# Performance work log

Measured on AMD Instinct MI355X. Metric: run time of the kernel, lower is better.

The kernel has to match this reference:

```python
import jax, jax.numpy as jnp
import numpy as np

B, N, E, H = 4, 4096, 1024, 16
D = E // H            # head_dim = 64
P_DIM = 64            # proj_dim; feature dim = 2*P_DIM = 128
EPS = 1e-4


def setup_inputs() -> dict:
    key = jax.random.key(0)
    ks = jax.random.split(key, 9)
    x = jax.random.normal(ks[0], (B, N, E), jnp.float32)
    init = 0.02
    Wq = jax.random.normal(ks[1], (E, E), jnp.float32) * init
    Wk = jax.random.normal(ks[2], (E, E), jnp.float32) * init
    Wv = jax.random.normal(ks[3], (E, E), jnp.float32) * init
    Wo = jax.random.normal(ks[4], (E, E), jnp.float32) * init
    bq = jnp.zeros((E,), jnp.float32)
    bk = jnp.zeros((E,), jnp.float32)
    bv = jnp.zeros((E,), jnp.float32)
    bo = jnp.zeros((E,), jnp.float32)
    # orthogonal random projection matrix (proj_dim, head_dim), fixed (non-trainable)
    g = np.random.default_rng(0).normal(size=(P_DIM, D))
    P = jnp.asarray(np.linalg.qr(g)[0], jnp.float32)
    return dict(x=x, Wq=Wq, bq=bq, Wk=Wk, bk=bk, Wv=Wv, bv=bv, Wo=Wo, bo=bo, P=P)


def _heads(z):
    # (B, N, E) -> (B, H, N, D)
    return z.reshape(B, N, H, D).transpose(0, 2, 1, 3)


def _normalize(z):
    return z / (jnp.linalg.norm(z, axis=-1, keepdims=True) + EPS)


def reference(x, Wq, bq, Wk, bk, Wv, bv, Wo, bo, P):
    q = _heads(x @ Wq.T + bq)
    k = _heads(x @ Wk.T + bk)
    v = _heads(x @ Wv.T + bv)
    q = _normalize(q)
    k = _normalize(k)
    scale = H ** 0.25
    qp = jnp.einsum('bhnd,ed->bhne', q, P) * scale
    kp = jnp.einsum('bhnd,ed->bhne', k, P) * scale
    fscale = P_DIM ** (-0.5)   # x.shape[-1]**-0.5 with last dim = proj_dim
    qf = jnp.concatenate([jnp.sin(qp), jnp.cos(qp)], axis=-1) * fscale  # (B,H,N,2p)
    kf = jnp.concatenate([jnp.sin(kp), jnp.cos(kp)], axis=-1) * fscale
    # non-causal linear attention: q @ (k^T v)
    kv = jnp.einsum('bhme,bhmd->bhed', kf, v)          # (B,H,2p,D)
    o = jnp.einsum('bhne,bhed->bhnd', qf, kv)          # (B,H,N,D)
    o = o.transpose(0, 2, 1, 3).reshape(B, N, E)
    return o @ Wo.T + bo
```

## Files before the change

kernel.cpp:

```cpp
#include <hip/hip_runtime.h>
#include <hip/hip_bf16.h>
#include <stdint.h>


typedef __bf16 bf16x8 __attribute__((ext_vector_type(8)));
typedef float f32x4 __attribute__((ext_vector_type(4)));

#define AS1 __attribute__((address_space(1)))
#define AS3 __attribute__((address_space(3)))

__device__ __forceinline__ void gl2lds16(const void* g, void* l) {
    __builtin_amdgcn_global_load_lds((const AS1 void*)g, (AS3 void*)l, 16, 0, 0);
}

static constexpr int GM = 16384, GN = 1024, GK = 1024;

__global__ void detect_kernel(const unsigned short* __restrict__ x,
                              int* __restrict__ flag) {
    __shared__ int s;
    const int lane = threadIdx.x;
    if (lane == 0) s = 0;
    __syncthreads();
    int cnt = 0;
#pragma unroll
    for (int i = 0; i < 2; ++i) {
        const unsigned short u = x[i * 64 + lane];
        const int e = (u >> 7) & 0xFF;
        cnt += (e >= 117 && e <= 131) ? 1 : 0;
    }
    atomicAdd(&s, cnt);
    __syncthreads();
    if (lane == 0) *flag = (s >= 100) ? 1 : 0;
}

__global__ __launch_bounds__(256) void cvt_kernel(
    const void* __restrict__ src, __hip_bfloat16* __restrict__ dst,
    int n, const int* __restrict__ flag) {
    if (*flag) return;
    const int i = (blockIdx.x * 256 + threadIdx.x) * 8;
    if (i >= n) return;
    const float* s = (const float*)src + i;
    const float4 a = *(const float4*)s;
    const float4 b = *(const float4*)(s + 4);
    union { uint4 u; __hip_bfloat16 h[8]; } pk;
    pk.h[0] = __float2bfloat16(a.x); pk.h[1] = __float2bfloat16(a.y);
    pk.h[2] = __float2bfloat16(a.z); pk.h[3] = __float2bfloat16(a.w);
    pk.h[4] = __float2bfloat16(b.x); pk.h[5] = __float2bfloat16(b.y);
    pk.h[6] = __float2bfloat16(b.z); pk.h[7] = __float2bfloat16(b.w);
    *(uint4*)(dst + i) = pk.u;
}

__global__ __launch_bounds__(256) void gemm1_kernel(
    const void* __restrict__ Adirect,
    const __hip_bfloat16* __restrict__ Acvt,
    const void* __restrict__ Wr, const __hip_bfloat16* __restrict__ Wc,
    const void* __restrict__ bias_raw,
    void* __restrict__ Cout,
    const int* __restrict__ flag, int last)
{
    __shared__ unsigned short smem[2 * 128 * 64];
    unsigned short* sA = smem;
    unsigned short* sB = smem + 128 * 64;

    const int tid  = threadIdx.x;
    const int lane = tid & 63;
    const int w    = tid >> 6;
    const int wm   = w >> 1, wn = w & 1;
    const int lr   = lane & 15, lk = lane >> 4;

    const int id    = blockIdx.x;
    const int xcd   = id & 7;
    const int slot  = id >> 3;
    const int m0    = (xcd * 16 + (slot & 15)) * 128;
    const int n0    = (slot >> 4) * 128;
    const int fl    = *flag;

    const __hip_bfloat16* A = fl ? (const __hip_bfloat16*)Adirect : Acvt;
    const __hip_bfloat16* W = fl ? (const __hip_bfloat16*)Wr : Wc;

    f32x4 acc[4][4];
#pragma unroll
    for (int i = 0; i < 4; ++i)
#pragma unroll
        for (int j = 0; j < 4; ++j)
            acc[i][j] = (f32x4){0.f, 0.f, 0.f, 0.f};

    const __hip_bfloat16* Ab = A + (size_t)m0 * GK;
    const __hip_bfloat16* Wb = W + (size_t)n0 * GK;

    for (int k0 = 0; k0 < GK; k0 += 64) {
#pragma unroll
        for (int j = 0; j < 4; ++j) {
            const int chunk = j * 256 + tid;
            const int row   = chunk >> 3;
            const int c     = chunk & 7;
            const int cs    = c ^ (row & 7);
            gl2lds16(Ab + (size_t)row * GK + k0 + cs * 8,
                     (char*)sA + (j * 256 + w * 64) * 16);
            gl2lds16(Wb + (size_t)row * GK + k0 + cs * 8,
                     (char*)sB + (j * 256 + w * 64) * 16);
        }
        __syncthreads();
#pragma unroll
        for (int kk = 0; kk < 64; kk += 32) {
            const int jj = ((kk >> 3) + lk) ^ (lr & 7);
            bf16x8 af[4], bfr[4];
#pragma unroll
            for (int i = 0; i < 4; ++i)
                af[i] = *(const bf16x8*)&sA[(wm * 64 + i * 16 + lr) * 64 + jj * 8];
#pragma unroll
            for (int j = 0; j < 4; ++j)
                bfr[j] = *(const bf16x8*)&sB[(wn * 64 + j * 16 + lr) * 64 + jj * 8];
#pragma unroll
            for (int i = 0; i < 4; ++i)
#pragma unroll
                for (int j = 0; j < 4; ++j)
                    acc[i][j] = __builtin_amdgcn_mfma_f32_16x16x32_bf16(
                        af[i], bfr[j], acc[i][j], 0, 0, 0);
        }
        __syncthreads();
    }

    const bool f32out = (last != 0) && (fl == 0);
    if (f32out) {
#pragma unroll
        for (int j = 0; j < 4; ++j) {
            const int col = n0 + wn * 64 + j * 16 + lr;
            const float bv = ((const float*)bias_raw)[col];
#pragma unroll
            for (int i = 0; i < 4; ++i) {
                const int rbase = m0 + wm * 64 + i * 16 + lk * 4;
#pragma unroll
                for (int r = 0; r < 4; ++r)
                    ((float*)Cout)[(size_t)(rbase + r) * GN + col] = acc[i][j][r] + bv;
            }
        }
        return;
    }
    __hip_bfloat16* sC = (__hip_bfloat16*)smem;
#pragma unroll
    for (int j = 0; j < 4; ++j) {
        const int col = wn * 64 + j * 16 + lr;
        const float bv = fl ? __bfloat162float(((const __hip_bfloat16*)bias_raw)[n0 + col])
                            : ((const float*)bias_raw)[n0 + col];
        const int c2 = col >> 3, o = col & 7;
#pragma unroll
        for (int i = 0; i < 4; ++i) {
            const int rb = wm * 64 + i * 16 + lk * 4;
#pragma unroll
            for (int r = 0; r < 4; ++r) {
                const int row = rb + r;
                sC[row * 128 + (c2 ^ (row & 7)) * 8 + o] = __float2bfloat16(acc[i][j][r] + bv);
            }
        }
    }
    __syncthreads();
    {
        const int row = tid >> 1, hf = tid & 1;
        __hip_bfloat16* dst = (__hip_bfloat16*)Cout + (size_t)(m0 + row) * GN + n0 + hf * 64;
#pragma unroll
        for (int q = 0; q < 8; ++q) {
            const int cc = (hf * 8 + q) ^ (row & 7);
            *(uint4*)(dst + q * 8) = *(const uint4*)&sC[row * 128 + cc * 8];
        }
    }
}

__global__ __launch_bounds__(256, 2) void gemm2_kernel(
    const void* __restrict__ Adirect,
    const __hip_bfloat16* __restrict__ Acvt,
    const void* __restrict__ W0r, const __hip_bfloat16* __restrict__ W0c,
    const void* __restrict__ W1r, const __hip_bfloat16* __restrict__ W1c,
    const void* __restrict__ b0r, const void* __restrict__ b1r,
    void* __restrict__ o0, void* __restrict__ o1,
    const int* __restrict__ flag)
{
    __shared__ unsigned short smem[3 * 128 * 64];
    unsigned short* sA  = smem;
    unsigned short* sB0 = smem + 128 * 64;
    unsigned short* sB1 = smem + 2 * 128 * 64;

    const int tid  = threadIdx.x;
    const int lane = tid & 63;
    const int w    = tid >> 6;
    const int wm   = w >> 1, wn = w & 1;
    const int lr   = lane & 15, lk = lane >> 4;

    const int id    = blockIdx.x;
    const int xcd   = id & 7;
    const int slot  = id >> 3;
    const int m0    = (xcd * 16 + (slot & 15)) * 128;
    const int n0    = (slot >> 4) * 128;
    const int fl    = *flag;

    const __hip_bfloat16* A  = fl ? (const __hip_bfloat16*)Adirect : Acvt;
    const __hip_bfloat16* W0 = fl ? (const __hip_bfloat16*)W0r : W0c;
    const __hip_bfloat16* W1 = fl ? (const __hip_bfloat16*)W1r : W1c;

    f32x4 acc[2][4][4];
#pragma unroll
    for (int t = 0; t < 2; ++t)
#pragma unroll
        for (int i = 0; i < 4; ++i)
#pragma unroll
            for (int j = 0; j < 4; ++j)
                acc[t][i][j] = (f32x4){0.f, 0.f, 0.f, 0.f};

    const __hip_bfloat16* Ab  = A + (size_t)m0 * GK;
    const __hip_bfloat16* W0b = W0 + (size_t)n0 * GK;
    const __hip_bfloat16* W1b = W1 + (size_t)n0 * GK;

    for (int k0 = 0; k0 < GK; k0 += 64) {
#pragma unroll
        for (int j = 0; j < 4; ++j) {
            const int chunk = j * 256 + tid;
            const int row   = chunk >> 3;
            const int c     = chunk & 7;
            const int cs    = c ^ (row & 7);
            const size_t go = (size_t)row * GK + k0 + cs * 8;
            const int lo = (j * 256 + w * 64) * 16;
            gl2lds16(Ab  + go, (char*)sA  + lo);
            gl2lds16(W0b + go, (char*)sB0 + lo);
            gl2lds16(W1b + go, (char*)sB1 + lo);
        }
        __syncthreads();
#pragma unroll
        for (int kk = 0; kk < 64; kk += 32) {
            const int jj = ((kk >> 3) + lk) ^ (lr & 7);
            bf16x8 af[4], b0f[4], b1f[4];
#pragma unroll
            for (int i = 0; i < 4; ++i)
                af[i] = *(const bf16x8*)&sA[(wm * 64 + i * 16 + lr) * 64 + jj * 8];
#pragma unroll
            for (int j = 0; j < 4; ++j)
                b0f[j] = *(const bf16x8*)&sB0[(wn * 64 + j * 16 + lr) * 64 + jj * 8];
#pragma unroll
            for (int j = 0; j < 4; ++j)
                b1f[j] = *(const bf16x8*)&sB1[(wn * 64 + j * 16 + lr) * 64 + jj * 8];
#pragma unroll
            for (int i = 0; i < 4; ++i)
#pragma unroll
                for (int j = 0; j < 4; ++j) {
                    acc[0][i][j] = __builtin_amdgcn_mfma_f32_16x16x32_bf16(
                        af[i], b0f[j], acc[0][i][j], 0, 0, 0);
                    acc[1][i][j] = __builtin_amdgcn_mfma_f32_16x16x32_bf16(
                        af[i], b1f[j], acc[1][i][j], 0, 0, 0);
                }
        }
        __syncthreads();
    }

    __hip_bfloat16* sC = (__hip_bfloat16*)smem;
#pragma unroll
    for (int t = 0; t < 2; ++t) {
        const void* bias_raw = t ? b1r : b0r;
        void* Cout = t ? o1 : o0;
#pragma unroll
        for (int j = 0; j < 4; ++j) {
            const int col = wn * 64 + j * 16 + lr;
            const float bv = fl ? __bfloat162float(((const __hip_bfloat16*)bias_raw)[n0 + col])
                                : ((const float*)bias_raw)[n0 + col];
            const int c2 = col >> 3, o = col & 7;
#pragma unroll
            for (int i = 0; i < 4; ++i) {
                const int rb = wm * 64 + i * 16 + lk * 4;
#pragma unroll
                for (int r = 0; r < 4; ++r) {
                    const int row = rb + r;
                    sC[row * 128 + (c2 ^ (row & 7)) * 8 + o] =
                        __float2bfloat16(acc[t][i][j][r] + bv);
                }
            }
        }
        __syncthreads();
        {
            const int row = tid >> 1, hf = tid & 1;
            __hip_bfloat16* dst = (__hip_bfloat16*)Cout + (size_t)(m0 + row) * GN + n0 + hf * 64;
#pragma unroll
            for (int q = 0; q < 8; ++q) {
                const int cc = (hf * 8 + q) ^ (row & 7);
                *(uint4*)(dst + q * 8) = *(const uint4*)&sC[row * 128 + cc * 8];
            }
        }
        __syncthreads();
    }
}

__device__ __forceinline__ void load_P(const void* Praw, int f,
                                       __hip_bfloat16* sP, int tid) {
    const int e = tid >> 2, q = tid & 3;
    union { uint4 u[2]; __hip_bfloat16 h[16]; } pk;
    if (f) {
        pk.u[0] = *(const uint4*)((const __hip_bfloat16*)Praw + e * 64 + q * 16);
        pk.u[1] = *(const uint4*)((const __hip_bfloat16*)Praw + e * 64 + q * 16 + 8);
    } else {
        const float* ps = (const float*)Praw + e * 64 + q * 16;
#pragma unroll
        for (int j = 0; j < 16; ++j) pk.h[j] = __float2bfloat16(ps[j]);
    }
    *(uint4*)&sP[e * 72 + q * 16]     = pk.u[0];
    *(uint4*)&sP[e * 72 + q * 16 + 8] = pk.u[1];
}

__device__ __forceinline__ float sumsq16(uint4 a, uint4 b) {
    union { uint4 u; __hip_bfloat16 h[8]; } x0, x1;
    x0.u = a; x1.u = b;
    float ss = 0.f;
#pragma unroll
    for (int j = 0; j < 8; ++j) {
        float v0 = __bfloat162float(x0.h[j]); ss += v0 * v0;
        float v1 = __bfloat162float(x1.h[j]); ss += v1 * v1;
    }
    return ss;
}

__global__ __launch_bounds__(256) void kv_kernel(
    const __hip_bfloat16* __restrict__ Km,
    const __hip_bfloat16* __restrict__ Vm,
    const void* __restrict__ Praw,
    float* __restrict__ gKV,
    const int* __restrict__ flag)
{
    __shared__ __hip_bfloat16 sK[64 * 72];
    __shared__ __hip_bfloat16 sVT[64 * 72];
    __shared__ __hip_bfloat16 sP[64 * 72];
    __shared__ __hip_bfloat16 sKFT[128 * 72];
    __shared__ float sRN[64];

    const int tid  = threadIdx.x;
    const int lane = tid & 63;
    const int w    = tid >> 6;
    const int lr   = lane & 15, lk = lane >> 4;
    const int bh   = blockIdx.y;
    const int b    = bh >> 4, h = bh & 15;
    const int nst  = blockIdx.x * 256;
    const int f    = *flag;
    const int n    = tid >> 2, q2 = tid & 3;

    load_P(Praw, f, sP, tid);

    f32x4 acck[2][4];
#pragma unroll
    for (int i = 0; i < 2; ++i)
#pragma unroll
        for (int j = 0; j < 4; ++j)
            acck[i][j] = (f32x4){0.f, 0.f, 0.f, 0.f};

    size_t base = ((size_t)(b * 4096 + nst + n)) * 1024 + h * 64 + q2 * 16;
    uint4 ka = *(const uint4*)(Km + base), kb = *(const uint4*)(Km + base + 8);
    uint4 va = *(const uint4*)(Vm + base), vb = *(const uint4*)(Vm + base + 8);

    for (int s = 0; s < 4; ++s) {
        __syncthreads();
        *(uint4*)&sK[n * 72 + q2 * 16]     = ka;
        *(uint4*)&sK[n * 72 + q2 * 16 + 8] = kb;
        {
            union { uint4 u[2]; __hip_bfloat16 h[16]; } vv;
            vv.u[0] = va; vv.u[1] = vb;
#pragma unroll
            for (int j = 0; j < 16; ++j) sVT[(q2 * 16 + j) * 72 + n] = vv.h[j];
        }
        {
            float ss = sumsq16(ka, kb);
            ss += __shfl_xor(ss, 1, 64);
            ss += __shfl_xor(ss, 2, 64);
            if (q2 == 0) sRN[n] = 2.0f / (sqrtf(ss) + 1e-4f);
        }
        if (s < 3) {
            base = ((size_t)(b * 4096 + nst + (s + 1) * 64 + n)) * 1024 + h * 64 + q2 * 16;
            ka = *(const uint4*)(Km + base); kb = *(const uint4*)(Km + base + 8);
            va = *(const uint4*)(Vm + base); vb = *(const uint4*)(Vm + base + 8);
        }
        {
            bf16x8 afr0 = *(const bf16x8*)&sK[(w * 16 + lr) * 72 + lk * 8];
            bf16x8 afr1 = *(const bf16x8*)&sK[(w * 16 + lr) * 72 + 32 + lk * 8];
            float rn[4];
#pragma unroll
            for (int r = 0; r < 4; ++r) rn[r] = sRN[w * 16 + lk * 4 + r];
#pragma unroll
            for (int eb = 0; eb < 4; ++eb) {
                f32x4 pa = (f32x4){0.f, 0.f, 0.f, 0.f};
                bf16x8 b0 = *(const bf16x8*)&sP[(eb * 16 + lr) * 72 + lk * 8];
                bf16x8 b1 = *(const bf16x8*)&sP[(eb * 16 + lr) * 72 + 32 + lk * 8];
                pa = __builtin_amdgcn_mfma_f32_16x16x32_bf16(afr0, b0, pa, 0, 0, 0);
                pa = __builtin_amdgcn_mfma_f32_16x16x32_bf16(afr1, b1, pa, 0, 0, 0);
                const int col = eb * 16 + lr;
#pragma unroll
                for (int r = 0; r < 4; ++r) {
                    const int row = w * 16 + lk * 4 + r;
                    float sv, cv;
                    __sincosf(pa[r] * rn[r], &sv, &cv);
                    sKFT[col * 72 + row]        = __float2bfloat16(sv * 0.125f);
                    sKFT[(col + 64) * 72 + row] = __float2bfloat16(cv * 0.125f);
                }
            }
        }
        __syncthreads();
#pragma unroll
        for (int ks = 0; ks < 2; ++ks) {
            bf16x8 a2[2], b2[4];
            a2[0] = *(const bf16x8*)&sKFT[(w * 16 + lr) * 72 + ks * 32 + lk * 8];
            a2[1] = *(const bf16x8*)&sKFT[((w + 4) * 16 + lr) * 72 + ks * 32 + lk * 8];
#pragma unroll
            for (int db = 0; db < 4; ++db)
                b2[db] = *(const bf16x8*)&sVT[(db * 16 + lr) * 72 + ks * 32 + lk * 8];
#pragma unroll
            for (int i = 0; i < 2; ++i)
#pragma unroll
                for (int db = 0; db < 4; ++db)
                    acck[i][db] = __builtin_amdgcn_mfma_f32_16x16x32_bf16(
                        a2[i], b2[db], acck[i][db], 0, 0, 0);
        }
    }

    float* out = gKV + (size_t)bh * 8192;
#pragma unroll
    for (int i = 0; i < 2; ++i)
#pragma unroll
        for (int db = 0; db < 4; ++db)
#pragma unroll
            for (int r = 0; r < 4; ++r) {
                const int e = (w + 4 * i) * 16 + lk * 4 + r;
                const int d = db * 16 + lr;
                atomicAdd(out + e * 64 + d, acck[i][db][r]);
            }
}

__global__ __launch_bounds__(256) void o_kernel(
    const __hip_bfloat16* __restrict__ Qm,
    const void* __restrict__ Praw,
    const float* __restrict__ gKV,
    __hip_bfloat16* __restrict__ O,
    const int* __restrict__ flag)
{
    __shared__ __hip_bfloat16 sQ[64 * 72];
    __shared__ __hip_bfloat16 sP[64 * 72];
    __shared__ __hip_bfloat16 sQF[64 * 136];
    __shared__ __hip_bfloat16 sKVT[64 * 136];
    __shared__ float sRN[64];

    const int tid  = threadIdx.x;
    const int lane = tid & 63;
    const int w    = tid >> 6;
    const int lr   = lane & 15, lk = lane >> 4;
    const int bh   = blockIdx.y;
    const int b    = bh >> 4, h = bh & 15;
    const int nst  = blockIdx.x * 256;
    const int f    = *flag;
    const int n    = tid >> 2, q2 = tid & 3;

    load_P(Praw, f, sP, tid);
    {
        const float* kvsrc = gKV + (size_t)bh * 8192;
        for (int t = tid; t < 8192; t += 256) {
            const int e = t >> 6, d = t & 63;
            sKVT[d * 136 + e] = __float2bfloat16(kvsrc[t]);
        }
    }

    size_t base = ((size_t)(b * 4096 + nst + n)) * 1024 + h * 64 + q2 * 16;
    uint4 qa = *(const uint4*)(Qm + base), qb = *(const uint4*)(Qm + base + 8);

    __syncthreads();

    for (int s = 0; s < 4; ++s) {
        const int gn0 = nst + s * 64;
        *(uint4*)&sQ[n * 72 + q2 * 16]     = qa;
        *(uint4*)&sQ[n * 72 + q2 * 16 + 8] = qb;
        {
            float ss = sumsq16(qa, qb);
            ss += __shfl_xor(ss, 1, 64);
            ss += __shfl_xor(ss, 2, 64);
            if (q2 == 0) sRN[n] = 2.0f / (sqrtf(ss) + 1e-4f);
        }
        if (s < 3) {
            base = ((size_t)(b * 4096 + nst + (s + 1) * 64 + n)) * 1024 + h * 64 + q2 * 16;
            qa = *(const uint4*)(Qm + base); qb = *(const uint4*)(Qm + base + 8);
        }
        {
            bf16x8 afr0 = *(const bf16x8*)&sQ[(w * 16 + lr) * 72 + lk * 8];
            bf16x8 afr1 = *(const bf16x8*)&sQ[(w * 16 + lr) * 72 + 32 + lk * 8];
            float rn[4];
#pragma unroll
            for (int r = 0; r < 4; ++r) rn[r] = sRN[w * 16 + lk * 4 + r];
#pragma unroll
            for (int eb = 0; eb < 4; ++eb) {
                f32x4 pa = (f32x4){0.f, 0.f, 0.f, 0.f};
                bf16x8 b0 = *(const bf16x8*)&sP[(eb * 16 + lr) * 72 + lk * 8];
                bf16x8 b1 = *(const bf16x8*)&sP[(eb * 16 + lr) * 72 + 32 + lk * 8];
                pa = __builtin_amdgcn_mfma_f32_16x16x32_bf16(afr0, b0, pa, 0, 0, 0);
                pa = __builtin_amdgcn_mfma_f32_16x16x32_bf16(afr1, b1, pa, 0, 0, 0);
                const int col = eb * 16 + lr;
#pragma unroll
                for (int r = 0; r < 4; ++r) {
                    const int row = w * 16 + lk * 4 + r;
                    float sv, cv;
                    __sincosf(pa[r] * rn[r], &sv, &cv);
                    sQF[row * 136 + col]      = __float2bfloat16(sv * 0.125f);
                    sQF[row * 136 + 64 + col] = __float2bfloat16(cv * 0.125f);
                }
            }
        }
        f32x4 oacc[4];
#pragma unroll
        for (int nb = 0; nb < 4; ++nb) oacc[nb] = (f32x4){0.f, 0.f, 0.f, 0.f};
#pragma unroll
        for (int ks = 0; ks < 4; ++ks) {
            bf16x8 aa = *(const bf16x8*)&sQF[(w * 16 + lr) * 136 + ks * 32 + lk * 8];
#pragma unroll
            for (int nb = 0; nb < 4; ++nb) {
                bf16x8 bb = *(const bf16x8*)&sKVT[(nb * 16 + lr) * 136 + ks * 32 + lk * 8];
                oacc[nb] = __builtin_amdgcn_mfma_f32_16x16x32_bf16(aa, bb, oacc[nb], 0, 0, 0);
            }
        }
#pragma unroll
        for (int nb = 0; nb < 4; ++nb)
#pragma unroll
            for (int r = 0; r < 4; ++r)
                sQ[(w * 16 + lk * 4 + r) * 72 + nb * 16 + lr] =
                    __float2bfloat16(oacc[nb][r]);
        {
            uint4 o0 = *(uint4*)&sQ[n * 72 + q2 * 16];
            uint4 o1 = *(uint4*)&sQ[n * 72 + q2 * 16 + 8];
            const size_t obase = ((size_t)(b * 4096 + gn0 + n)) * 1024 + h * 64 + q2 * 16;
            *(uint4*)(O + obase)     = o0;
            *(uint4*)(O + obase + 8) = o1;
        }
    }
}

extern "C" void kernel_launch(void* const* d_in, const int* in_sizes, int n_in,
                              void* d_out, int out_size, void* d_ws, size_t ws_size,
                              hipStream_t stream)
{
    (void)in_sizes; (void)n_in; (void)out_size; (void)ws_size;
    const void* x  = d_in[0];
    const void* Wq = d_in[1];
    const void* bq = d_in[2];
    const void* Wk = d_in[3];
    const void* bk = d_in[4];
    const void* Wv = d_in[5];
    const void* bv = d_in[6];
    const void* Wo = d_in[7];
    const void* bo = d_in[8];
    const void* P  = d_in[9];

    constexpr size_t XE = (size_t)GM * GN;
    constexpr size_t WE = (size_t)GN * GK;
    constexpr size_t KVE = (size_t)64 * 128 * 64;

    __hip_bfloat16* xb  = (__hip_bfloat16*)d_ws;
    __hip_bfloat16* wqb = xb + XE;
    __hip_bfloat16* wkb = wqb + WE;
    __hip_bfloat16* wvb = wkb + WE;
    __hip_bfloat16* wob = wvb + WE;
    __hip_bfloat16* R1  = wob + WE;
    __hip_bfloat16* R2  = R1 + XE;
    float* gKV = (float*)(R2 + XE);
    int* flag  = (int*)(gKV + KVE);

    dim3 blk(256);
    hipLaunchKernelGGL(detect_kernel, dim3(1), dim3(64), 0, stream,
                       (const unsigned short*)x, flag);
    hipMemsetAsync(gKV, 0, KVE * sizeof(float), stream);

    hipLaunchKernelGGL(cvt_kernel, dim3(8192), blk, 0, stream, x,  xb,  (int)XE, flag);
    hipLaunchKernelGGL(cvt_kernel, dim3(512),  blk, 0, stream, Wq, wqb, (int)WE, flag);
    hipLaunchKernelGGL(cvt_kernel, dim3(512),  blk, 0, stream, Wk, wkb, (int)WE, flag);
    hipLaunchKernelGGL(cvt_kernel, dim3(512),  blk, 0, stream, Wv, wvb, (int)WE, flag);
    hipLaunchKernelGGL(cvt_kernel, dim3(512),  blk, 0, stream, Wo, wob, (int)WE, flag);

    hipLaunchKernelGGL(gemm2_kernel, dim3(1024), blk, 0, stream,
                       x, xb, Wk, wkb, Wv, wvb, bk, bv, R1, R2, flag);
    hipLaunchKernelGGL(kv_kernel, dim3(16, 64), blk, 0, stream, R1, R2, P, gKV, flag);
    hipLaunchKernelGGL(gemm1_kernel, dim3(1024), blk, 0, stream,
                       x, xb, Wq, wqb, bq, R2, flag, 0);
    hipLaunchKernelGGL(o_kernel, dim3(16, 64), blk, 0, stream, R2, P, gKV, R1, flag);
    hipLaunchKernelGGL(gemm1_kernel, dim3(1024), blk, 0, stream,
                       R1, R1, Wo, wob, bo, d_out, flag, 1);
}
```

Baseline: 404.5 us.

## Use 256x128 tiles in single GEMMs and replace KV atomics with slab reduction

```diff
diff --git a/kernel.cpp b/kernel.cpp
--- a/kernel.cpp
+++ b/kernel.cpp
@@ -14,6 +14,7 @@
 }
 
 static constexpr int GM = 16384, GN = 1024, GK = 1024;
+static constexpr int KV_SLABS = 8;
 
 __global__ void detect_kernel(const unsigned short* __restrict__ x,
                               int* __restrict__ flag) {
@@ -50,7 +51,7 @@
     *(uint4*)(dst + i) = pk.u;
 }
 
-__global__ __launch_bounds__(256) void gemm1_kernel(
+__global__ __launch_bounds__(256, 2) void gemm1m2_kernel(
     const void* __restrict__ Adirect,
     const __hip_bfloat16* __restrict__ Acvt,
     const void* __restrict__ Wr, const __hip_bfloat16* __restrict__ Wc,
@@ -58,9 +59,10 @@
     void* __restrict__ Cout,
     const int* __restrict__ flag, int last)
 {
-    __shared__ unsigned short smem[2 * 128 * 64];
-    unsigned short* sA = smem;
-    unsigned short* sB = smem + 128 * 64;
+    __shared__ unsigned short smem[3 * 128 * 64];
+    unsigned short* sA0 = smem;
+    unsigned short* sA1 = smem + 128 * 64;
+    unsigned short* sB  = smem + 2 * 128 * 64;
 
     const int tid  = threadIdx.x;
     const int lane = tid & 63;
@@ -68,25 +70,28 @@
     const int wm   = w >> 1, wn = w & 1;
     const int lr   = lane & 15, lk = lane >> 4;
 
-    const int id    = blockIdx.x;
-    const int xcd   = id & 7;
-    const int slot  = id >> 3;
-    const int m0    = (xcd * 16 + (slot & 15)) * 128;
-    const int n0    = (slot >> 4) * 128;
-    const int fl    = *flag;
+    const int id   = blockIdx.x;
+    const int xcd  = id & 7;
+    const int s    = id >> 3;
+    const int m0   = (xcd * 8 + (s & 7)) * 256;
+    const int n0   = (s >> 3) * 128;
+    const int fl   = *flag;
 
     const __hip_bfloat16* A = fl ? (const __hip_bfloat16*)Adirect : Acvt;
     const __hip_bfloat16* W = fl ? (const __hip_bfloat16*)Wr : Wc;
 
-    f32x4 acc[4][4];
-#pragma unroll
-    for (int i = 0; i < 4; ++i)
-#pragma unroll
-        for (int j = 0; j < 4; ++j)
-            acc[i][j] = (f32x4){0.f, 0.f, 0.f, 0.f};
-
-    const __hip_bfloat16* Ab = A + (size_t)m0 * GK;
-    const __hip_bfloat16* Wb = W + (size_t)n0 * GK;
+    f32x4 acc[2][4][4];
+#pragma unroll
+    for (int t = 0; t < 2; ++t)
+#pragma unroll
+        for (int i = 0; i < 4; ++i)
+#pragma unroll
+            for (int j = 0; j < 4; ++j)
+                acc[t][i][j] = (f32x4){0.f, 0.f, 0.f, 0.f};
+
+    const __hip_bfloat16* Ab0 = A + (size_t)m0 * GK;
+    const __hip_bfloat16* Ab1 = A + (size_t)(m0 + 128) * GK;
+    const __hip_bfloat16* Wb  = W + (size_t)n0 * GK;
 
     for (int k0 = 0; k0 < GK; k0 += 64) {
 #pragma unroll
@@ -95,28 +100,35 @@
             const int row   = chunk >> 3;
             const int c     = chunk & 7;
             const int cs    = c ^ (row & 7);
-            gl2lds16(Ab + (size_t)row * GK + k0 + cs * 8,
-                     (char*)sA + (j * 256 + w * 64) * 16);
-            gl2lds16(Wb + (size_t)row * GK + k0 + cs * 8,
-                     (char*)sB + (j * 256 + w * 64) * 16);
+            const size_t go = (size_t)row * GK + k0 + cs * 8;
+            const int lo = (j * 256 + w * 64) * 16;
+            gl2lds16(Ab0 + go, (char*)sA0 + lo);
+            gl2lds16(Ab1 + go, (char*)sA1 + lo);
+            gl2lds16(Wb  + go, (char*)sB  + lo);
         }
         __syncthreads();
 #pragma unroll
         for (int kk = 0; kk < 64; kk += 32) {
             const int jj = ((kk >> 3) + lk) ^ (lr & 7);
-            bf16x8 af[4], bfr[4];
+            bf16x8 a0f[4], a1f[4], bfr[4];
 #pragma unroll
             for (int i = 0; i < 4; ++i)
-                af[i] = *(const bf16x8*)&sA[(wm * 64 + i * 16 + lr) * 64 + jj * 8];
+                a0f[i] = *(const bf16x8*)&sA0[(wm * 64 + i * 16 + lr) * 64 + jj * 8];
+#pragma unroll
+            for (int i = 0; i < 4; ++i)
+                a1f[i] = *(const bf16x8*)&sA1[(wm * 64 + i * 16 + lr) * 64 + jj * 8];
 #pragma unroll
             for (int j = 0; j < 4; ++j)
                 bfr[j] = *(const bf16x8*)&sB[(wn * 64 + j * 16 + lr) * 64 + jj * 8];
 #pragma unroll
             for (int i = 0; i < 4; ++i)
 #pragma unroll
-                for (int j = 0; j < 4; ++j)
-                    acc[i][j] = __builtin_amdgcn_mfma_f32_16x16x32_bf16(
-                        af[i], bfr[j], acc[i][j], 0, 0, 0);
+                for (int j = 0; j < 4; ++j) {
+                    acc[0][i][j] = __builtin_amdgcn_mfma_f32_16x16x32_bf16(
+                        a0f[i], bfr[j], acc[0][i][j], 0, 0, 0);
+                    acc[1][i][j] = __builtin_amdgcn_mfma_f32_16x16x32_bf16(
+                        a1f[i], bfr[j], acc[1][i][j], 0, 0, 0);
+                }
         }
         __syncthreads();
     }
@@ -124,45 +136,53 @@
     const bool f32out = (last != 0) && (fl == 0);
     if (f32out) {
 #pragma unroll
+        for (int t = 0; t < 2; ++t)
+#pragma unroll
+            for (int j = 0; j < 4; ++j) {
+                const int col = n0 + wn * 64 + j * 16 + lr;
+                const float bv = ((const float*)bias_raw)[col];
+#pragma unroll
+                for (int i = 0; i < 4; ++i) {
+                    const int rbase = m0 + t * 128 + wm * 64 + i * 16 + lk * 4;
+#pragma unroll
+                    for (int r = 0; r < 4; ++r)
+                        ((float*)Cout)[(size_t)(rbase + r) * GN + col] = acc[t][i][j][r] + bv;
+                }
+            }
+        return;
+    }
+    __hip_bfloat16* sC = (__hip_bfloat16*)smem;
+#pragma unroll
+    for (int t = 0; t < 2; ++t) {
+#pragma unroll
         for (int j = 0; j < 4; ++j) {
-            const int col = n0 + wn * 64 + j * 16 + lr;
-            const float bv = ((const float*)bias_raw)[col];
+            const int col = wn * 64 + j * 16 + lr;
+            const float bv = fl ? __bfloat162float(((const __hip_bfloat16*)bias_raw)[n0 + col])
+                                : ((const float*)bias_raw)[n0 + col];
+            const int c2 = col >> 3, o = col & 7;
 #pragma unroll
             for (int i = 0; i < 4; ++i) {
-                const int rbase = m0 + wm * 64 + i * 16 + lk * 4;
-#pragma unroll
-                for (int r = 0; r < 4; ++r)
-                    ((float*)Cout)[(size_t)(rbase + r) * GN + col] = acc[i][j][r] + bv;
-            }
-        }
-        return;
-    }
-    __hip_bfloat16* sC = (__hip_bfloat16*)smem;
-#pragma unroll
-    for (int j = 0; j < 4; ++j) {
-        const int col = wn * 64 + j * 16 + lr;
-        const float bv = fl ? __bfloat162float(((const __hip_bfloat16*)bias_raw)[n0 + col])
-                            : ((const float*)bias_raw)[n0 + col];
-        const int c2 = col >> 3, o = col & 7;
-#pragma unroll
-        for (int i = 0; i < 4; ++i) {
-            const int rb = wm * 64 + i * 16 + lk * 4;
-#pragma unroll
-            for (int r = 0; r < 4; ++r) {
-                const int row = rb + r;
-                sC[row * 128 + (c2 ^ (row & 7)) * 8 + o] = __float2bfloat16(acc[i][j][r] + bv);
-            }
-        }
-    }
-    __syncthreads();
-    {
-        const int row = tid >> 1, hf = tid & 1;
-        __hip_bfloat16* dst = (__hip_bfloat16*)Cout + (size_t)(m0 + row) * GN + n0 + hf * 64;
-#pragma unroll
-        for (int q = 0; q < 8; ++q) {
-            const int cc = (hf * 8 + q) ^ (row & 7);
-            *(uint4*)(dst + q * 8) = *(const uint4*)&sC[row * 128 + cc * 8];
-        }
+                const int rb = wm * 64 + i * 16 + lk * 4;
+#pragma unroll
+                for (int r = 0; r < 4; ++r) {
+                    const int row = rb + r;
+                    sC[row * 128 + (c2 ^ (row & 7)) * 8 + o] =
+                        __float2bfloat16(acc[t][i][j][r] + bv);
+                }
+            }
+        }
+        __syncthreads();
+        {
+            const int row = tid >> 1, hf = tid & 1;
+            __hip_bfloat16* dst = (__hip_bfloat16*)Cout +
+                (size_t)(m0 + t * 128 + row) * GN + n0 + hf * 64;
+#pragma unroll
+            for (int q = 0; q < 8; ++q) {
+                const int cc = (hf * 8 + q) ^ (row & 7);
+                *(uint4*)(dst + q * 8) = *(const uint4*)&sC[row * 128 + cc * 8];
+            }
+        }
+        __syncthreads();
     }
 }
 
@@ -318,7 +338,7 @@
     const __hip_bfloat16* __restrict__ Km,
     const __hip_bfloat16* __restrict__ Vm,
     const void* __restrict__ Praw,
-    float* __restrict__ gKV,
+    float* __restrict__ PKV,
     const int* __restrict__ flag)
 {
     __shared__ __hip_bfloat16 sK[64 * 72];
@@ -333,7 +353,7 @@
     const int lr   = lane & 15, lk = lane >> 4;
     const int bh   = blockIdx.y;
     const int b    = bh >> 4, h = bh & 15;
-    const int nst  = blockIdx.x * 256;
+    const int nst  = blockIdx.x * 512;
     const int f    = *flag;
     const int n    = tid >> 2, q2 = tid & 3;
 
@@ -350,7 +370,7 @@
     uint4 ka = *(const uint4*)(Km + base), kb = *(const uint4*)(Km + base + 8);
     uint4 va = *(const uint4*)(Vm + base), vb = *(const uint4*)(Vm + base + 8);
 
-    for (int s = 0; s < 4; ++s) {
+    for (int s = 0; s < 8; ++s) {
         __syncthreads();
         *(uint4*)&sK[n * 72 + q2 * 16]     = ka;
         *(uint4*)&sK[n * 72 + q2 * 16 + 8] = kb;
@@ -366,7 +386,7 @@
             ss += __shfl_xor(ss, 2, 64);
             if (q2 == 0) sRN[n] = 2.0f / (sqrtf(ss) + 1e-4f);
         }
-        if (s < 3) {
+        if (s < 7) {
             base = ((size_t)(b * 4096 + nst + (s + 1) * 64 + n)) * 1024 + h * 64 + q2 * 16;
             ka = *(const uint4*)(Km + base); kb = *(const uint4*)(Km + base + 8);
             va = *(const uint4*)(Vm + base); vb = *(const uint4*)(Vm + base + 8);
@@ -413,7 +433,7 @@
         }
     }
 
-    float* out = gKV + (size_t)bh * 8192;
+    float* out = PKV + ((size_t)blockIdx.x * 64 + bh) * 8192;
 #pragma unroll
     for (int i = 0; i < 2; ++i)
 #pragma unroll
@@ -422,8 +442,21 @@
             for (int r = 0; r < 4; ++r) {
                 const int e = (w + 4 * i) * 16 + lk * 4 + r;
                 const int d = db * 16 + lr;
-                atomicAdd(out + e * 64 + d, acck[i][db][r]);
-            }
+                out[e * 64 + d] = acck[i][db][r];
+            }
+}
+
+__global__ __launch_bounds__(256) void kv_reduce_kernel(
+    const float* __restrict__ PKV, float* __restrict__ gKV)
+{
+    const int i = (blockIdx.x * 256 + threadIdx.x) * 4;
+    f32x4 s = (f32x4){0.f, 0.f, 0.f, 0.f};
+#pragma unroll
+    for (int sl = 0; sl < KV_SLABS; ++sl) {
+        const float4 v = *(const float4*)(PKV + (size_t)sl * 64 * 8192 + i);
+        s[0] += v.x; s[1] += v.y; s[2] += v.z; s[3] += v.w;
+    }
+    *(float4*)(gKV + i) = *(float4*)&s;
 }
 
 __global__ __launch_bounds__(256) void o_kernel(
@@ -557,12 +590,12 @@
     __hip_bfloat16* R1  = wob + WE;
     __hip_bfloat16* R2  = R1 + XE;
     float* gKV = (float*)(R2 + XE);
-    int* flag  = (int*)(gKV + KVE);
+    float* PKV = gKV + KVE;
+    int* flag  = (int*)(PKV + (size_t)KV_SLABS * 64 * 8192);
 
     dim3 blk(256);
     hipLaunchKernelGGL(detect_kernel, dim3(1), dim3(64), 0, stream,
                        (const unsigned short*)x, flag);
-    hipMemsetAsync(gKV, 0, KVE * sizeof(float), stream);
 
     hipLaunchKernelGGL(cvt_kernel, dim3(8192), blk, 0, stream, x,  xb,  (int)XE, flag);
     hipLaunchKernelGGL(cvt_kernel, dim3(512),  blk, 0, stream, Wq, wqb, (int)WE, flag);
@@ -572,10 +605,11 @@
 
     hipLaunchKernelGGL(gemm2_kernel, dim3(1024), blk, 0, stream,
                        x, xb, Wk, wkb, Wv, wvb, bk, bv, R1, R2, flag);
-    hipLaunchKernelGGL(kv_kernel, dim3(16, 64), blk, 0, stream, R1, R2, P, gKV, flag);
-    hipLaunchKernelGGL(gemm1_kernel, dim3(1024), blk, 0, stream,
+    hipLaunchKernelGGL(kv_kernel, dim3(KV_SLABS, 64), blk, 0, stream, R1, R2, P, PKV, flag);
+    hipLaunchKernelGGL(kv_reduce_kernel, dim3(512), blk, 0, stream, PKV, gKV);
+    hipLaunchKernelGGL(gemm1m2_kernel, dim3(512), blk, 0, stream,
                        x, xb, Wq, wqb, bq, R2, flag, 0);
     hipLaunchKernelGGL(o_kernel, dim3(16, 64), blk, 0, stream, R2, P, gKV, R1, flag);
-    hipLaunchKernelGGL(gemm1_kernel, dim3(1024), blk, 0, stream,
+    hipLaunchKernelGGL(gemm1m2_kernel, dim3(512), blk, 0, stream,
                        R1, R1, Wo, wob, bo, d_out, flag, 1);
 }
```

New measurement: 362.5 us. 10.4% less time.
